# Optimization experiments

Hardware: AMD Instinct MI355X
Metric: run time of the kernel (lower is better)

The kernel has to match this reference:

```python
import jax, jax.numpy as jnp
import numpy as np

N, E, D_IN, D_H, D_OUT = 50000, 800000, 64, 64, 64


def _lin_params(key, d_in, d_out, bias=True, scale=0.05):
    kw, kb = jax.random.split(key)
    W = jax.random.normal(kw, (d_in, d_out), dtype=jnp.float32) * scale
    if bias:
        b = jax.random.normal(kb, (d_out,), dtype=jnp.float32) * scale
        return W, b
    return (W,)


def setup_inputs() -> dict:
    key = jax.random.key(0)
    ks = jax.random.split(key, 12)
    x = jax.random.normal(ks[0], (N, D_IN), dtype=jnp.float32)
    edge_index = jax.random.randint(ks[1], (2, E), 0, N, dtype=jnp.int64)
    edge_attr = jax.random.normal(ks[2], (E, 1), dtype=jnp.float32)
    Wq1, bq1 = _lin_params(ks[3], D_IN, D_H)
    Wk1, bk1 = _lin_params(ks[4], D_IN, D_H)
    Wv1, bv1 = _lin_params(ks[5], D_IN, D_H)
    (We1,) = _lin_params(ks[6], 1, D_H, bias=False)
    Ws1, bs1 = _lin_params(ks[7], D_IN, D_H)
    Wq2, bq2 = _lin_params(ks[8], D_H, D_OUT)
    Wk2, bk2 = _lin_params(ks[9], D_H, D_OUT)
    Wv2, bv2 = _lin_params(ks[10], D_H, D_OUT)
    (We2,) = _lin_params(jax.random.fold_in(key, 100), 1, D_OUT, bias=False)
    Ws2, bs2 = _lin_params(ks[11], D_H, D_OUT)
    return dict(x=x, edge_index=edge_index, edge_attr=edge_attr,
                Wq1=Wq1, bq1=bq1, Wk1=Wk1, bk1=bk1, Wv1=Wv1, bv1=bv1, We1=We1, Ws1=Ws1, bs1=bs1,
                Wq2=Wq2, bq2=bq2, Wk2=Wk2, bk2=bk2, Wv2=Wv2, bv2=bv2, We2=We2, Ws2=Ws2, bs2=bs2)


def transformer_conv(x, src, dst, edge_attr, Wq, bq, Wk, bk, Wv, bv, We, Ws, bs):
    # PyG TransformerConv, heads=1, concat=False, root_weight=True, edge_dim=1
    d = Wq.shape[1]
    n = x.shape[0]
    q = x @ Wq + bq                       # [N, d]
    e = edge_attr @ We                    # [E, d] edge-conditioned term
    k = x[src] @ Wk + bk + e              # [E, d] gather source features
    v = x[src] @ Wv + bv + e              # [E, d]
    score = jnp.sum(q[dst] * k, axis=-1) / jnp.sqrt(jnp.asarray(d, x.dtype))  # [E]
    # segment softmax over incoming edges of each target node
    m = jax.ops.segment_max(score, dst, num_segments=n)
    a = jnp.exp(score - m[dst])
    denom = jax.ops.segment_sum(a, dst, num_segments=n)
    alpha = a / denom[dst]
    out = jax.ops.segment_sum(alpha[:, None] * v, dst, num_segments=n)  # [N, d]
    return out + x @ Ws + bs              # root/skip connection


def reference(x, edge_index, edge_attr,
              Wq1, bq1, Wk1, bk1, Wv1, bv1, We1, Ws1, bs1,
              Wq2, bq2, Wk2, bk2, Wv2, bv2, We2, Ws2, bs2):
    src, dst = edge_index[0], edge_index[1]
    h = transformer_conv(x, src, dst, edge_attr, Wq1, bq1, Wk1, bk1, Wv1, bv1, We1, Ws1, bs1)
    h = jax.nn.relu(h)
    out = transformer_conv(h, src, dst, edge_attr, Wq2, bq2, Wk2, bk2, Wv2, bv2, We2, Ws2, bs2)
    return out
```

## Files before the change

### kernel.cpp

```cpp
#include <hip/hip_runtime.h>
#include <hip/hip_bf16.h>
#include <hip/hip_fp16.h>

typedef short bshort8 __attribute__((ext_vector_type(8)));
typedef float f32x4 __attribute__((ext_vector_type(4)));
typedef unsigned short ushort8v __attribute__((ext_vector_type(8)));

__device__ __forceinline__ int clampi(int v, int lo, int hi) {
    return v < lo ? lo : (v > hi ? hi : v);
}
__device__ __forceinline__ ushort f2bf(float f) {
    uint u = __float_as_uint(f);
    return (ushort)((u + 0x7FFFu + ((u >> 16) & 1u)) >> 16);
}
__device__ __forceinline__ float bf2f(ushort b) { return __uint_as_float(((uint)b) << 16); }

__device__ __forceinline__ float dot8(float4 qA, float4 qB, ushort8v k8) {
    return qA.x * bf2f(k8[0]) + qA.y * bf2f(k8[1]) + qA.z * bf2f(k8[2]) + qA.w * bf2f(k8[3])
         + qB.x * bf2f(k8[4]) + qB.y * bf2f(k8[5]) + qB.z * bf2f(k8[6]) + qB.w * bf2f(k8[7]);
}

__device__ __forceinline__ uint pack_edge(int src, float ea) {
    ushort h = __half_as_ushort(__float2half(ea));
    return ((uint)src << 15) | ((uint)(h >> 1) & 0x7FFFu);
}
__device__ __forceinline__ int rec_src(uint r) { return (int)(r >> 15); }
__device__ __forceinline__ float rec_ea(uint r) {
    return __half2float(__ushort_as_half((ushort)((r & 0x7FFFu) << 1)));
}

__global__ void pack_and_zero(const float* __restrict__ Wq1, const float* __restrict__ Wk1,
                              const float* __restrict__ Wv1, const float* __restrict__ Ws1,
                              const float* __restrict__ Wq2, const float* __restrict__ Wk2,
                              const float* __restrict__ Wv2, const float* __restrict__ Ws2,
                              ushort* __restrict__ Bp1, ushort* __restrict__ Bp2,
                              int* __restrict__ count, int n) {
    if (blockIdx.x >= 16) {
        int j = (blockIdx.x - 16) * 256 + threadIdx.x;
        if (j < n) count[j] = 0;
        return;
    }
    int tid = blockIdx.x * 256 + threadIdx.x;
    int layer = tid >> 11;
    int t2 = tid & 2047;
    int lane = t2 & 63;
    int th = t2 >> 6;
    int h = th & 1, t = th >> 1;
    const float* W = layer ? ((t < 4) ? Wq2 : (t < 8) ? Wk2 : (t < 12) ? Wv2 : Ws2)
                           : ((t < 4) ? Wq1 : (t < 8) ? Wk1 : (t < 12) ? Wv1 : Ws1);
    ushort* Bp = layer ? Bp2 : Bp1;
    int col = ((t & 3) << 4) + (lane & 15);
    int g = lane >> 4;
    #pragma unroll
    for (int i = 0; i < 8; ++i) {
        int k = 32 * h + 16 * (i >> 2) + 4 * g + (i & 3);
        Bp[t2 * 8 + i] = f2bf(W[k * 64 + col]);
    }
}

__global__ void hist_kernel(const int* __restrict__ ei, int* __restrict__ count,
                            int* __restrict__ rank, int E, int n) {
    int j = blockIdx.x * blockDim.x + threadIdx.x;
    if (j < E) {
        int d = clampi(ei[E + j], 0, n - 1);
        rank[j] = atomicAdd(&count[d], 1);
    }
}

__global__ void scan_exclusive(const int* __restrict__ count, int* __restrict__ row_ptr,
                               int n) {
    __shared__ int wsum[16];
    int tid = threadIdx.x, lane = tid & 63, wv = tid >> 6;
    int carry = 0;
    for (int base = 0; base < n; base += 4096) {
        int i4 = base + tid * 4;
        int v0 = 0, v1 = 0, v2 = 0, v3 = 0;
        if (i4 + 3 < n) {
            int4 t = *(const int4*)(count + i4);
            v0 = t.x; v1 = t.y; v2 = t.z; v3 = t.w;
        } else {
            if (i4     < n) v0 = count[i4];
            if (i4 + 1 < n) v1 = count[i4 + 1];
            if (i4 + 2 < n) v2 = count[i4 + 2];
            if (i4 + 3 < n) v3 = count[i4 + 3];
        }
        int s0 = v0, s1 = s0 + v1, s2 = s1 + v2, s3 = s2 + v3;
        int sv = s3;
        #pragma unroll
        for (int off = 1; off < 64; off <<= 1) {
            int t = __shfl_up(sv, off, 64);
            if (lane >= off) sv += t;
        }
        if (lane == 63) wsum[wv] = sv;
        __syncthreads();
        if (tid < 16) {
            int ws = wsum[tid];
            #pragma unroll
            for (int off = 1; off < 16; off <<= 1) {
                int t = __shfl_up(ws, off, 64);
                if (tid >= off) ws += t;
            }
            wsum[tid] = ws;
        }
        __syncthreads();
        int add = carry + (wv ? wsum[wv - 1] : 0) + (sv - s3);
        if (i4     < n) row_ptr[i4]     = add;
        if (i4 + 1 < n) row_ptr[i4 + 1] = add + s0;
        if (i4 + 2 < n) row_ptr[i4 + 2] = add + s1;
        if (i4 + 3 < n) row_ptr[i4 + 3] = add + s2;
        carry += wsum[15];
        __syncthreads();
    }
    if (tid == 0) row_ptr[n] = carry;
}

__global__ void scatter_kernel(const int* __restrict__ ei, const float* __restrict__ ea,
                               const int* __restrict__ rank, const int* __restrict__ row_ptr,
                               uint* __restrict__ cse, int E, int n) {
    int j = blockIdx.x * blockDim.x + threadIdx.x;
    if (j < E) {
        int d = clampi(ei[E + j], 0, n - 1);
        int pos = row_ptr[d] + rank[j];
        if (pos >= 0 && pos < E)
            cse[pos] = pack_edge(clampi(ei[j], 0, n - 1), ea[j]);
    }
}

template<bool INF32>
__global__ __launch_bounds__(256) void node_transform_mfma(
    const void* __restrict__ xin, const ushort* __restrict__ Bpack,
    const float* __restrict__ We,
    const float* __restrict__ bq, const float* __restrict__ bk,
    const float* __restrict__ bv, const float* __restrict__ bs,
    ushort* __restrict__ Qb, ushort* __restrict__ KVb,
    float* __restrict__ S, float* __restrict__ qWe, int n)
{
    __shared__ bshort8 Blds[2048];
    {
        const bshort8* gB = (const bshort8*)Bpack;
        for (int i = threadIdx.x; i < 2048; i += 256) Blds[i] = gB[i];
    }
    __syncthreads();

    int lane = threadIdx.x & 63;
    int wv = threadIdx.x >> 6;
    int tile = blockIdx.x * 4 + wv;
    int ntiles = (n + 15) >> 4;
    if (tile >= ntiles) return;
    int r0 = tile << 4;
    int c = lane & 15, g = lane >> 4;

    int arow = r0 + c; if (arow >= n) arow = n - 1;
    union { ushort4 u[2]; bshort8 v; } A0, A1;
    if constexpr (INF32) {
        const float* xr = (const float*)xin + (size_t)arow * 64 + 4 * g;
        float4 f0 = *(const float4*)(xr);
        float4 f1 = *(const float4*)(xr + 16);
        float4 f2 = *(const float4*)(xr + 32);
        float4 f3 = *(const float4*)(xr + 48);
        A0.u[0] = make_ushort4(f2bf(f0.x), f2bf(f0.y), f2bf(f0.z), f2bf(f0.w));
        A0.u[1] = make_ushort4(f2bf(f1.x), f2bf(f1.y), f2bf(f1.z), f2bf(f1.w));
        A1.u[0] = make_ushort4(f2bf(f2.x), f2bf(f2.y), f2bf(f2.z), f2bf(f2.w));
        A1.u[1] = make_ushort4(f2bf(f3.x), f2bf(f3.y), f2bf(f3.z), f2bf(f3.w));
    } else {
        const ushort* xr = (const ushort*)xin + (size_t)arow * 64 + 4 * g;
        A0.u[0] = *(const ushort4*)(xr);
        A0.u[1] = *(const ushort4*)(xr + 16);
        A1.u[0] = *(const ushort4*)(xr + 32);
        A1.u[1] = *(const ushort4*)(xr + 48);
    }

    f32x4 acc[16];
    #pragma unroll
    for (int t = 0; t < 16; ++t) acc[t] = (f32x4){0.f, 0.f, 0.f, 0.f};
    #pragma unroll
    for (int t = 0; t < 16; ++t) {
        acc[t] = __builtin_amdgcn_mfma_f32_16x16x32_bf16(A0.v, Blds[(2 * t) * 64 + lane], acc[t], 0, 0, 0);
        acc[t] = __builtin_amdgcn_mfma_f32_16x16x32_bf16(A1.v, Blds[(2 * t + 1) * 64 + lane], acc[t], 0, 0, 0);
    }

    float we_c[4], bq_c[4];
    #pragma unroll
    for (int t = 0; t < 4; ++t) { we_c[t] = We[16 * t + c]; bq_c[t] = bq[16 * t + c]; }
    #pragma unroll
    for (int j = 0; j < 4; ++j) {
        float part = 0.f;
        #pragma unroll
        for (int t = 0; t < 4; ++t) part += (acc[t][j] + bq_c[t]) * we_c[t];
        part += __shfl_xor(part, 1);
        part += __shfl_xor(part, 2);
        part += __shfl_xor(part, 4);
        part += __shfl_xor(part, 8);
        int orow = r0 + 4 * g + j;
        if (c == 0 && orow < n) qWe[orow] = part;
    }

    #pragma unroll
    for (int tt = 0; tt < 4; ++tt) {
        int col = 16 * tt + c;
        float vbk = bk[col], vbv = bv[col], vbs = bs[col];
        #pragma unroll
        for (int j = 0; j < 4; ++j) {
            int orow = r0 + 4 * g + j;
            if (orow >= n) continue;
            size_t o = (size_t)orow * 64 + col;
            Qb[o] = f2bf(acc[tt][j] + bq_c[tt]);
            KVb[(size_t)orow * 128 + col]      = f2bf(acc[4 + tt][j] + vbk);
            KVb[(size_t)orow * 128 + 64 + col] = f2bf(acc[8 + tt][j] + vbv);
            S[o] = acc[12 + tt][j] + vbs;
        }
    }
}

template<int L1>
__global__ __launch_bounds__(256) void agg3_kernel(
    const ushort* __restrict__ Qb, const ushort* __restrict__ KVb,
    const float* __restrict__ S, const float* __restrict__ qWe,
    const float* __restrict__ We, const int* __restrict__ row_ptr,
    const uint* __restrict__ cse, void* __restrict__ outp, int n, int E)
{
    int q8 = threadIdx.x & 7;
    int gid = (blockIdx.x * blockDim.x + threadIdx.x) >> 3;
    int ng  = (gridDim.x * blockDim.x) >> 3;
    float4 weA = ((const float4*)We)[2 * q8];
    float4 weB = ((const float4*)We)[2 * q8 + 1];

    for (int i = gid; i < n; i += ng) {
        int beg = clampi(row_ptr[i], 0, E);
        int end = clampi(row_ptr[i + 1], beg, E);
        ushort8v q8v = *(const ushort8v*)(Qb + (size_t)i * 64 + 8 * q8);
        float4 qA = make_float4(bf2f(q8v[0]), bf2f(q8v[1]), bf2f(q8v[2]), bf2f(q8v[3]));
        float4 qB = make_float4(bf2f(q8v[4]), bf2f(q8v[5]), bf2f(q8v[6]), bf2f(q8v[7]));
        float qwe8 = qWe[i] * 0.125f;
        f32x4 aA = {0.f, 0.f, 0.f, 0.f}, aB = {0.f, 0.f, 0.f, 0.f};
        float ssum = 0.f, sea = 0.f;

        int e = beg;
        for (; e + 2 <= end; e += 2) {
            uint ed0 = cse[e], ed1 = cse[e + 1];
            const ushort* r0 = KVb + (size_t)clampi(rec_src(ed0), 0, n - 1) * 128 + 8 * q8;
            const ushort* r1 = KVb + (size_t)clampi(rec_src(ed1), 0, n - 1) * 128 + 8 * q8;
            ushort8v k0 = *(const ushort8v*)(r0);
            ushort8v v0 = *(const ushort8v*)(r0 + 64);
            ushort8v k1 = *(const ushort8v*)(r1);
            ushort8v v1 = *(const ushort8v*)(r1 + 64);
            float ea0 = rec_ea(ed0), ea1 = rec_ea(ed1);
            float d0 = dot8(qA, qB, k0);
            float d1 = dot8(qA, qB, k1);
            d0 += __shfl_xor(d0, 1); d1 += __shfl_xor(d1, 1);
            d0 += __shfl_xor(d0, 2); d1 += __shfl_xor(d1, 2);
            d0 += __shfl_xor(d0, 4); d1 += __shfl_xor(d1, 4);
            float p0 = __expf(fmaf(ea0, qwe8, d0 * 0.125f));
            float p1 = __expf(fmaf(ea1, qwe8, d1 * 0.125f));
            ssum += p0 + p1;
            sea = fmaf(p0, ea0, fmaf(p1, ea1, sea));
            aA[0] = fmaf(p0, bf2f(v0[0]), fmaf(p1, bf2f(v1[0]), aA[0]));
            aA[1] = fmaf(p0, bf2f(v0[1]), fmaf(p1, bf2f(v1[1]), aA[1]));
            aA[2] = fmaf(p0, bf2f(v0[2]), fmaf(p1, bf2f(v1[2]), aA[2]));
            aA[3] = fmaf(p0, bf2f(v0[3]), fmaf(p1, bf2f(v1[3]), aA[3]));
            aB[0] = fmaf(p0, bf2f(v0[4]), fmaf(p1, bf2f(v1[4]), aB[0]));
            aB[1] = fmaf(p0, bf2f(v0[5]), fmaf(p1, bf2f(v1[5]), aB[1]));
            aB[2] = fmaf(p0, bf2f(v0[6]), fmaf(p1, bf2f(v1[6]), aB[2]));
            aB[3] = fmaf(p0, bf2f(v0[7]), fmaf(p1, bf2f(v1[7]), aB[3]));
        }
        if (e < end) {
            uint ed = cse[e];
            const ushort* row = KVb + (size_t)clampi(rec_src(ed), 0, n - 1) * 128 + 8 * q8;
            ushort8v k0 = *(const ushort8v*)(row);
            ushort8v v0 = *(const ushort8v*)(row + 64);
            float ea0 = rec_ea(ed);
            float d0 = dot8(qA, qB, k0);
            d0 += __shfl_xor(d0, 1);
            d0 += __shfl_xor(d0, 2);
            d0 += __shfl_xor(d0, 4);
            float p0 = __expf(fmaf(ea0, qwe8, d0 * 0.125f));
            ssum += p0;
            sea = fmaf(p0, ea0, sea);
            aA[0] = fmaf(p0, bf2f(v0[0]), aA[0]);
            aA[1] = fmaf(p0, bf2f(v0[1]), aA[1]);
            aA[2] = fmaf(p0, bf2f(v0[2]), aA[2]);
            aA[3] = fmaf(p0, bf2f(v0[3]), aA[3]);
            aB[0] = fmaf(p0, bf2f(v0[4]), aB[0]);
            aB[1] = fmaf(p0, bf2f(v0[5]), aB[1]);
            aB[2] = fmaf(p0, bf2f(v0[6]), aB[2]);
            aB[3] = fmaf(p0, bf2f(v0[7]), aB[3]);
        }

        float inv = (ssum > 0.f) ? 1.f / ssum : 0.f;
        float eawe = sea * inv;
        const float4* Srow = (const float4*)(S + (size_t)i * 64);
        float4 sA = Srow[2 * q8], sB = Srow[2 * q8 + 1];
        float o0 = fmaf(aA[0], inv, fmaf(eawe, weA.x, sA.x));
        float o1 = fmaf(aA[1], inv, fmaf(eawe, weA.y, sA.y));
        float o2 = fmaf(aA[2], inv, fmaf(eawe, weA.z, sA.z));
        float o3 = fmaf(aA[3], inv, fmaf(eawe, weA.w, sA.w));
        float o4 = fmaf(aB[0], inv, fmaf(eawe, weB.x, sB.x));
        float o5 = fmaf(aB[1], inv, fmaf(eawe, weB.y, sB.y));
        float o6 = fmaf(aB[2], inv, fmaf(eawe, weB.z, sB.z));
        float o7 = fmaf(aB[3], inv, fmaf(eawe, weB.w, sB.w));
        if (L1) {
            o0 = fmaxf(o0, 0.f); o1 = fmaxf(o1, 0.f); o2 = fmaxf(o2, 0.f); o3 = fmaxf(o3, 0.f);
            o4 = fmaxf(o4, 0.f); o5 = fmaxf(o5, 0.f); o6 = fmaxf(o6, 0.f); o7 = fmaxf(o7, 0.f);
            union { ushort u[8]; ushort8v v; } ov;
            ov.u[0] = f2bf(o0); ov.u[1] = f2bf(o1); ov.u[2] = f2bf(o2); ov.u[3] = f2bf(o3);
            ov.u[4] = f2bf(o4); ov.u[5] = f2bf(o5); ov.u[6] = f2bf(o6); ov.u[7] = f2bf(o7);
            *(ushort8v*)((ushort*)outp + (size_t)i * 64 + 8 * q8) = ov.v;
        } else {
            float4* Or = (float4*)((float*)outp + (size_t)i * 64);
            Or[2 * q8]     = make_float4(o0, o1, o2, o3);
            Or[2 * q8 + 1] = make_float4(o4, o5, o6, o7);
        }
    }
}

extern "C" void kernel_launch(void* const* d_in, const int* in_sizes, int n_in,
                              void* d_out, int out_size, void* d_ws, size_t ws_size,
                              hipStream_t stream) {
    const float* x   = (const float*)d_in[0];
    const int*   ei  = (const int*)d_in[1];
    const float* ea  = (const float*)d_in[2];
    const float *Wq1 = (const float*)d_in[3],  *bq1 = (const float*)d_in[4];
    const float *Wk1 = (const float*)d_in[5],  *bk1 = (const float*)d_in[6];
    const float *Wv1 = (const float*)d_in[7],  *bv1 = (const float*)d_in[8];
    const float *We1 = (const float*)d_in[9];
    const float *Ws1 = (const float*)d_in[10], *bs1 = (const float*)d_in[11];
    const float *Wq2 = (const float*)d_in[12], *bq2 = (const float*)d_in[13];
    const float *Wk2 = (const float*)d_in[14], *bk2 = (const float*)d_in[15];
    const float *Wv2 = (const float*)d_in[16], *bv2 = (const float*)d_in[17];
    const float *We2 = (const float*)d_in[18];
    const float *Ws2 = (const float*)d_in[19], *bs2 = (const float*)d_in[20];

    const int N_ = in_sizes[0] / 64;
    const int E_ = in_sizes[2];

    char* wsb = (char*)d_ws;
    size_t off = 0;
    auto carve = [&](size_t bytes) -> void* {
        void* p = (void*)(wsb + off);
        off += (bytes + 255) & ~(size_t)255;
        return p;
    };
    ushort* Qb   = (ushort*)carve((size_t)N_ * 64 * 2);
    float*  S    = (float*)carve((size_t)N_ * 64 * 4);
    ushort* KVb  = (ushort*)carve((size_t)N_ * 128 * 2);
    ushort* hb   = (ushort*)carve((size_t)N_ * 64 * 2);
    float*  qWe  = (float*)carve((size_t)N_ * 4);
    int*    count   = (int*)carve((size_t)N_ * 4);
    int*    row_ptr = (int*)carve((size_t)(N_ + 1) * 4);
    int*    rank    = (int*)carve((size_t)E_ * 4);
    uint*   cse     = (uint*)carve((size_t)E_ * 4);
    ushort* Bp1     = (ushort*)carve(2048 * 8 * 2);
    ushort* Bp2     = (ushort*)carve(2048 * 8 * 2);
    (void)ws_size; (void)n_in; (void)out_size;

    pack_and_zero<<<16 + (N_ + 255) / 256, 256, 0, stream>>>(
        Wq1, Wk1, Wv1, Ws1, Wq2, Wk2, Wv2, Ws2, Bp1, Bp2, count, N_);

    hist_kernel<<<(E_ + 255) / 256, 256, 0, stream>>>(ei, count, rank, E_, N_);
    scan_exclusive<<<1, 1024, 0, stream>>>(count, row_ptr, N_);
    scatter_kernel<<<(E_ + 255) / 256, 256, 0, stream>>>(ei, ea, rank, row_ptr, cse, E_, N_);

    int ntb = (((N_ + 15) / 16) + 3) / 4;

    node_transform_mfma<true><<<ntb, 256, 0, stream>>>(x, Bp1, We1, bq1, bk1, bv1, bs1,
                                                       Qb, KVb, S, qWe, N_);
    agg3_kernel<1><<<1568, 256, 0, stream>>>(Qb, KVb, S, qWe, We1, row_ptr, cse, hb, N_, E_);
    node_transform_mfma<false><<<ntb, 256, 0, stream>>>(hb, Bp2, We2, bq2, bk2, bv2, bs2,
                                                        Qb, KVb, S, qWe, N_);
    agg3_kernel<0><<<1568, 256, 0, stream>>>(Qb, KVb, S, qWe, We2, row_ptr, cse, d_out, N_, E_);
}
```

Baseline: 194.9 us.

## Sort nodes by degree for aggregation and stage node-transform stores through LDS

Adds a degree-bucketing pass (histogram, scan, scatter over clamped in-degree) that builds a node order array. The aggregation kernel then walks nodes in that order, so that 8-lane groups within a wave handle nodes of similar degree and divergence is reduced. Separately, the node transform writes its Q/KV/S tiles into padded shared memory and then stores them to global memory as coalesced 16-byte vectors instead of scattered scalar writes. The cost is three extra small launches, a loss of locality for the Q/S/output accesses in the aggregation kernel, and more shared memory per block, which can lower occupancy.

```diff
diff --git a/kernel.cpp b/kernel.cpp
--- a/kernel.cpp
+++ b/kernel.cpp
@@ -34,10 +34,11 @@
                               const float* __restrict__ Wq2, const float* __restrict__ Wk2,
                               const float* __restrict__ Wv2, const float* __restrict__ Ws2,
                               ushort* __restrict__ Bp1, ushort* __restrict__ Bp2,
-                              int* __restrict__ count, int n) {
+                              int* __restrict__ count, int* __restrict__ dcount, int n) {
     if (blockIdx.x >= 16) {
         int j = (blockIdx.x - 16) * 256 + threadIdx.x;
         if (j < n) count[j] = 0;
+        if (blockIdx.x == 16 && threadIdx.x < 64) dcount[threadIdx.x] = 0;
         return;
     }
     int tid = blockIdx.x * 256 + threadIdx.x;
@@ -126,6 +127,41 @@
     }
 }
 
+__global__ void deg_hist(const int* __restrict__ row_ptr, int* __restrict__ dcount,
+                         int* __restrict__ nrank, int n) {
+    int i = blockIdx.x * blockDim.x + threadIdx.x;
+    if (i < n) {
+        int deg = clampi(row_ptr[i + 1] - row_ptr[i], 0, 63);
+        nrank[i] = atomicAdd(&dcount[deg], 1);
+    }
+}
+
+__global__ void dscan_kernel(const int* __restrict__ dcount, int* __restrict__ dbase) {
+    int lane = threadIdx.x;
+    int v = dcount[lane];
+    int sv = v;
+    #pragma unroll
+    for (int off = 1; off < 64; off <<= 1) {
+        int t = __shfl_up(sv, off, 64);
+        if (lane >= off) sv += t;
+    }
+    dbase[lane] = sv - v;
+}
+
+__global__ void dscatter_kernel(const int* __restrict__ row_ptr, const int* __restrict__ dbase,
+                                const int* __restrict__ nrank, int* __restrict__ order, int n) {
+    int i = blockIdx.x * blockDim.x + threadIdx.x;
+    if (i < n) {
+        int deg = clampi(row_ptr[i + 1] - row_ptr[i], 0, 63);
+        int pos = dbase[deg] + nrank[i];
+        if (pos >= 0 && pos < n) order[pos] = i;
+    }
+}
+
+#define QT_STRIDE 72
+#define KV_STRIDE 136
+#define ST_STRIDE 68
+
 template<bool INF32>
 __global__ __launch_bounds__(256) void node_transform_mfma(
     const void* __restrict__ xin, const ushort* __restrict__ Bpack,
@@ -136,6 +172,9 @@
     float* __restrict__ S, float* __restrict__ qWe, int n)
 {
     __shared__ bshort8 Blds[2048];
+    __shared__ ushort qlds[4 * 16 * QT_STRIDE];
+    __shared__ ushort kvlds[4 * 16 * KV_STRIDE];
+    __shared__ float  slds[4 * 16 * ST_STRIDE];
     {
         const bshort8* gB = (const bshort8*)Bpack;
         for (int i = threadIdx.x; i < 2048; i += 256) Blds[i] = gB[i];
@@ -195,20 +234,46 @@
         if (c == 0 && orow < n) qWe[orow] = part;
     }
 
+    ushort* qt = qlds + wv * 16 * QT_STRIDE;
+    ushort* kt = kvlds + wv * 16 * KV_STRIDE;
+    float*  st = slds + wv * 16 * ST_STRIDE;
     #pragma unroll
     for (int tt = 0; tt < 4; ++tt) {
         int col = 16 * tt + c;
         float vbk = bk[col], vbv = bv[col], vbs = bs[col];
         #pragma unroll
         for (int j = 0; j < 4; ++j) {
-            int orow = r0 + 4 * g + j;
-            if (orow >= n) continue;
-            size_t o = (size_t)orow * 64 + col;
-            Qb[o] = f2bf(acc[tt][j] + bq_c[tt]);
-            KVb[(size_t)orow * 128 + col]      = f2bf(acc[4 + tt][j] + vbk);
-            KVb[(size_t)orow * 128 + 64 + col] = f2bf(acc[8 + tt][j] + vbv);
-            S[o] = acc[12 + tt][j] + vbs;
-        }
+            int row = 4 * g + j;
+            qt[row * QT_STRIDE + col]      = f2bf(acc[tt][j] + bq_c[tt]);
+            kt[row * KV_STRIDE + col]      = f2bf(acc[4 + tt][j] + vbk);
+            kt[row * KV_STRIDE + 64 + col] = f2bf(acc[8 + tt][j] + vbv);
+            st[row * ST_STRIDE + col]      = acc[12 + tt][j] + vbs;
+        }
+    }
+
+    #pragma unroll
+    for (int k2 = 0; k2 < 2; ++k2) {
+        int ch = k2 * 64 + lane;
+        int row = ch >> 3, off = ch & 7;
+        if (r0 + row < n)
+            *(ushort8v*)(Qb + (size_t)(r0 + row) * 64 + off * 8) =
+                *(const ushort8v*)(qt + row * QT_STRIDE + off * 8);
+    }
+    #pragma unroll
+    for (int k4 = 0; k4 < 4; ++k4) {
+        int ch = k4 * 64 + lane;
+        int row = ch >> 4, off = ch & 15;
+        if (r0 + row < n)
+            *(ushort8v*)(KVb + (size_t)(r0 + row) * 128 + off * 8) =
+                *(const ushort8v*)(kt + row * KV_STRIDE + off * 8);
+    }
+    #pragma unroll
+    for (int k4 = 0; k4 < 4; ++k4) {
+        int ch = k4 * 64 + lane;
+        int row = ch >> 4, off = ch & 15;
+        if (r0 + row < n)
+            *(float4*)(S + (size_t)(r0 + row) * 64 + off * 4) =
+                *(const float4*)(st + row * ST_STRIDE + off * 4);
     }
 }
 
@@ -217,7 +282,8 @@
     const ushort* __restrict__ Qb, const ushort* __restrict__ KVb,
     const float* __restrict__ S, const float* __restrict__ qWe,
     const float* __restrict__ We, const int* __restrict__ row_ptr,
-    const uint* __restrict__ cse, void* __restrict__ outp, int n, int E)
+    const uint* __restrict__ cse, const int* __restrict__ order,
+    void* __restrict__ outp, int n, int E)
 {
     int q8 = threadIdx.x & 7;
     int gid = (blockIdx.x * blockDim.x + threadIdx.x) >> 3;
@@ -225,7 +291,8 @@
     float4 weA = ((const float4*)We)[2 * q8];
     float4 weB = ((const float4*)We)[2 * q8 + 1];
 
-    for (int i = gid; i < n; i += ng) {
+    for (int ii = gid; ii < n; ii += ng) {
+        int i = clampi(order[ii], 0, n - 1);
         int beg = clampi(row_ptr[i], 0, E);
         int end = clampi(row_ptr[i + 1], beg, E);
         ushort8v q8v = *(const ushort8v*)(Qb + (size_t)i * 64 + 8 * q8);
@@ -349,23 +416,33 @@
     int*    row_ptr = (int*)carve((size_t)(N_ + 1) * 4);
     int*    rank    = (int*)carve((size_t)E_ * 4);
     uint*   cse     = (uint*)carve((size_t)E_ * 4);
+    int*    nrank   = (int*)carve((size_t)N_ * 4);
+    int*    order   = (int*)carve((size_t)N_ * 4);
+    int*    dcount  = (int*)carve(64 * 4);
+    int*    dbase   = (int*)carve(64 * 4);
     ushort* Bp1     = (ushort*)carve(2048 * 8 * 2);
     ushort* Bp2     = (ushort*)carve(2048 * 8 * 2);
     (void)ws_size; (void)n_in; (void)out_size;
 
     pack_and_zero<<<16 + (N_ + 255) / 256, 256, 0, stream>>>(
-        Wq1, Wk1, Wv1, Ws1, Wq2, Wk2, Wv2, Ws2, Bp1, Bp2, count, N_);
+        Wq1, Wk1, Wv1, Ws1, Wq2, Wk2, Wv2, Ws2, Bp1, Bp2, count, dcount, N_);
 
     hist_kernel<<<(E_ + 255) / 256, 256, 0, stream>>>(ei, count, rank, E_, N_);
     scan_exclusive<<<1, 1024, 0, stream>>>(count, row_ptr, N_);
     scatter_kernel<<<(E_ + 255) / 256, 256, 0, stream>>>(ei, ea, rank, row_ptr, cse, E_, N_);
 
+    deg_hist<<<(N_ + 255) / 256, 256, 0, stream>>>(row_ptr, dcount, nrank, N_);
+    dscan_kernel<<<1, 64, 0, stream>>>(dcount, dbase);
+    dscatter_kernel<<<(N_ + 255) / 256, 256, 0, stream>>>(row_ptr, dbase, nrank, order, N_);
+
     int ntb = (((N_ + 15) / 16) + 3) / 4;
 
     node_transform_mfma<true><<<ntb, 256, 0, stream>>>(x, Bp1, We1, bq1, bk1, bv1, bs1,
                                                        Qb, KVb, S, qWe, N_);
-    agg3_kernel<1><<<1568, 256, 0, stream>>>(Qb, KVb, S, qWe, We1, row_ptr, cse, hb, N_, E_);
+    agg3_kernel<1><<<1568, 256, 0, stream>>>(Qb, KVb, S, qWe, We1, row_ptr, cse, order,
+                                             hb, N_, E_);
     node_transform_mfma<false><<<ntb, 256, 0, stream>>>(hb, Bp2, We2, bq2, bk2, bv2, bs2,
                                                         Qb, KVb, S, qWe, N_);
-    agg3_kernel<0><<<1568, 256, 0, stream>>>(Qb, KVb, S, qWe, We2, row_ptr, cse, d_out, N_, E_);
-}
+    agg3_kernel<0><<<1568, 256, 0, stream>>>(Qb, KVb, S, qWe, We2, row_ptr, cse, order,
+                                             d_out, N_, E_);
+}
```

Result: slower. 324.2 us (+66.3%).
